# Kernel optimization log

Hardware: AMD Instinct MI355X
Metric: run time of the kernel (lower is better)

Reference implementation:

```python
import jax, jax.numpy as jnp
import numpy as np


def _analytic_phase(x):
    """FFT-based analytic-signal phase, mean over channels. x: (B, C, T) -> (B, T)."""
    B, C, T = x.shape
    Xf = jnp.fft.fft(x, axis=-1)  # complex64
    # Hilbert multiplier: h[0]=1, h[1:T//2]=2, h[T//2]=1 (T even), rest 0
    h = np.zeros((T,), dtype=np.float32)
    h[0] = 1.0
    h[1:T // 2] = 2.0
    if T % 2 == 0:
        h[T // 2] = 1.0
    analytic = jnp.fft.ifft(Xf * jnp.asarray(h), axis=-1)
    phase = jnp.angle(analytic)          # (B, C, T)
    return phase.mean(axis=1)            # (B, T)


def setup_inputs() -> dict:
    key = jax.random.key(0)
    k = jax.random.split(key, 6)
    B, C, T = 32, 9, 4096
    num_codes, code_dim = 512, 64
    half = code_dim // 2
    s = 1.0 / np.sqrt(C)  # kaiming-uniform-ish scale for Linear(9, .)
    return {
        "imu_signal": jax.random.normal(k[0], (B, C, T), dtype=jnp.float32),
        "W_mag": jax.random.uniform(k[1], (half, C), jnp.float32, -s, s),
        "b_mag": jax.random.uniform(k[2], (half,), jnp.float32, -s, s),
        "W_phase": jax.random.uniform(k[3], (half, C), jnp.float32, -s, s),
        "b_phase": jax.random.uniform(k[4], (half,), jnp.float32, -s, s),
        "codebook": jax.random.normal(k[5], (num_codes, code_dim), dtype=jnp.float32),
    }


def reference(imu_signal, W_mag, b_mag, W_phase, b_phase, codebook):
    # imu_signal: (B, 9, T)
    phases = _analytic_phase(imu_signal)                      # (B, T)
    imu_btc = jnp.transpose(imu_signal, (0, 2, 1))            # (B, T, 9)

    mag_features = imu_btc @ W_mag.T + b_mag                  # (B, T, 32)

    phase_input = jnp.stack([jnp.cos(phases), jnp.sin(phases)], axis=-1)  # (B, T, 2)
    combined = jnp.concatenate([imu_btc[:, :, :7], phase_input], axis=-1)  # (B, T, 9)
    phase_features = combined @ W_phase.T + b_phase           # (B, T, 32)

    features = jnp.concatenate([mag_features, phase_features], axis=-1)  # (B, T, 64)

    # cdist argmin == argmin of squared distances: ||f||^2 - 2 f.c + ||c||^2
    d2 = (jnp.sum(features * features, axis=-1, keepdims=True)
          - 2.0 * jnp.einsum("btd,kd->btk", features, codebook)
          + jnp.sum(codebook * codebook, axis=-1))            # (B, T, K)
    indices = jnp.argmin(d2, axis=-1)                         # (B, T)
    quantized = codebook[indices]                             # (B, T, 64)
    return quantized, indices, phases
```

## Files before the change

kernel.cpp:

```cpp
#include <hip/hip_runtime.h>
#include <math.h>

#define TN 4096
#define HN 2048
#define NB 32
#define NCH 9
#define NCODES 512
#define CDIM 64
#define TAU 1e-3f
#define PTS 128
#define CHK 64
#define NCHK 8

typedef _Float16 f16x8 __attribute__((ext_vector_type(8)));
typedef float f32x4 __attribute__((ext_vector_type(4)));

__device__ __forceinline__ float2 cmulf(float2 a, float2 b) {
    return make_float2(a.x * b.x - a.y * b.y, a.x * b.y + a.y * b.x);
}
__device__ __forceinline__ float2 f2add(float2 a, float2 b) {
    return make_float2(a.x + b.x, a.y + b.y);
}
__device__ __forceinline__ float2 f2sub(float2 a, float2 b) {
    return make_float2(a.x - b.x, a.y - b.y);
}

__device__ __forceinline__ unsigned long long packsi(float s, int i) {
    unsigned u = __float_as_uint(s);
    u = (u & 0x80000000u) ? ~u : (u | 0x80000000u);
    return ((unsigned long long)u << 32) | (unsigned)i;
}
__device__ __forceinline__ float unpacks(unsigned long long v) {
    unsigned u = (unsigned)(v >> 32);
    u = (u & 0x80000000u) ? (u & 0x7fffffffu) : ~u;
    return __uint_as_float(u);
}

__device__ __forceinline__ void gload_lds16(const void* g, void* l) {
    __builtin_amdgcn_global_load_lds(
        (const __attribute__((address_space(1))) unsigned int*)g,
        (__attribute__((address_space(3))) unsigned int*)l, 16, 0, 0);
}

__device__ __forceinline__ size_t aunit(int pbase, int plane, int s, int hi16, int l15) {
    return ((size_t)(((pbase * 2 + plane) * 2 + s) * 4 + hi16) << 4) + l15;
}

__global__ __launch_bounds__(256) void prep_kernel(const float* __restrict__ cb,
                                                   float* __restrict__ cn,
                                                   f16x8* __restrict__ cbswz,
                                                   float* __restrict__ ph) {
    const int bid = blockIdx.x;
    const int tid = threadIdx.x;
    if (bid < 512) {
        ph[bid * 256 + tid] = 0.0f;
        return;
    }
    if (bid < 544) {
        const int u = (bid - 512) * 256 + tid;
        const int k = u >> 4;
        const int j = u & 15;
        const int ob = j ^ (k & 15);
        const int plane = ob >> 3;
        const int d0 = (ob & 7) * 8;
        f16x8 out;
        #pragma unroll
        for (int e = 0; e < 8; ++e) {
            float c = cb[k * CDIM + d0 + e];
            _Float16 hh = (_Float16)c;
            out[e] = plane ? (_Float16)(c - (float)hh) : hh;
        }
        cbswz[u] = out;
        return;
    }
    for (int k = tid; k < NCODES; k += 256) {
        const float4* c4 = (const float4*)(cb + (size_t)k * CDIM);
        float s = 0.0f;
        #pragma unroll
        for (int q = 0; q < 16; ++q) {
            float4 c = c4[q];
            s = fmaf(c.x, c.x, s);
            s = fmaf(c.y, c.y, s);
            s = fmaf(c.z, c.z, s);
            s = fmaf(c.w, c.w, s);
        }
        cn[k] = s;
    }
}

#define HT 512
__global__ __launch_bounds__(HT) void hilbert_phase_kernel(
    const float* __restrict__ x, float* __restrict__ phases) {
    __shared__ float2 bufA[TN];
    __shared__ float2 bufB[TN];
    __shared__ float2 tw[HN];
    const int tid = threadIdx.x;
    const int row1 = 2 * blockIdx.x;
    const int row2 = row1 + 1;
    const int b1 = row1 / NCH;
    const int b2 = row2 / NCH;
    const float* xr1 = x + (size_t)row1 * TN;
    const float* xr2 = x + (size_t)row2 * TN;

    for (int i = tid; i < HN; i += HT) {
        float ang = -3.14159265358979323846f * ((float)i / (float)HN);
        float s, c;
        sincosf(ang, &s, &c);
        tw[i] = make_float2(c, s);
    }
    for (int i = tid; i < TN; i += HT) {
        bufA[i] = make_float2(xr1[i], xr2[i]);
    }
    __syncthreads();

    float2* src = bufA;
    float2* dst = bufB;
    for (int stage = 0; stage < 6; ++stage) {
        const int m = 1 << (2 * stage);
        for (int idx = tid; idx < 1024; idx += HT) {
            const int kk = idx & (m - 1);
            const int jm = idx - kk;
            float2 a0 = src[idx];
            float2 a1 = src[idx + 1024];
            float2 a2 = src[idx + 2048];
            float2 a3 = src[idx + 3072];
            float2 b0 = f2add(a0, a2);
            float2 b1 = f2add(a1, a3);
            float2 b2 = f2sub(a0, a2);
            float2 b3 = f2sub(a1, a3);
            float2 w1 = tw[jm];
            float2 w2 = tw[2 * jm];
            float2 w3 = cmulf(w1, w2);
            float2 y0 = f2add(b0, b1);
            float2 mi = make_float2(b2.x + b3.y, b2.y - b3.x);
            float2 pi_ = make_float2(b2.x - b3.y, b2.y + b3.x);
            dst[4 * jm + kk]         = y0;
            dst[4 * jm + kk + m]     = cmulf(mi, w1);
            dst[4 * jm + kk + 2 * m] = cmulf(f2sub(b0, b1), w2);
            dst[4 * jm + kk + 3 * m] = cmulf(pi_, w3);
        }
        __syncthreads();
        float2* t0 = src; src = dst; dst = t0;
    }
    const float inv = 1.0f / (float)TN;
    for (int i = tid; i < TN; i += HT) {
        float sc;
        if (i == 0 || i == HN) sc = inv;
        else if (i < HN) sc = 2.0f * inv;
        else sc = 0.0f;
        float2 v = src[i];
        v.x *= sc; v.y *= sc;
        src[i] = v;
    }
    __syncthreads();
    for (int stage = 0; stage < 6; ++stage) {
        const int m = 1 << (2 * stage);
        for (int idx = tid; idx < 1024; idx += HT) {
            const int kk = idx & (m - 1);
            const int jm = idx - kk;
            float2 a0 = src[idx];
            float2 a1 = src[idx + 1024];
            float2 a2 = src[idx + 2048];
            float2 a3 = src[idx + 3072];
            float2 b0 = f2add(a0, a2);
            float2 b1 = f2add(a1, a3);
            float2 b2 = f2sub(a0, a2);
            float2 b3 = f2sub(a1, a3);
            float2 w1 = tw[jm];      w1.y = -w1.y;
            float2 w2 = tw[2 * jm];  w2.y = -w2.y;
            float2 w3 = cmulf(w1, w2);
            float2 y0 = f2add(b0, b1);
            float2 pi_ = make_float2(b2.x - b3.y, b2.y + b3.x);
            float2 mi = make_float2(b2.x + b3.y, b2.y - b3.x);
            dst[4 * jm + kk]         = y0;
            dst[4 * jm + kk + m]     = cmulf(pi_, w1);
            dst[4 * jm + kk + 2 * m] = cmulf(f2sub(b0, b1), w2);
            dst[4 * jm + kk + 3 * m] = cmulf(mi, w3);
        }
        __syncthreads();
        float2* t0 = src; src = dst; dst = t0;
    }
    float* ph1 = phases + (size_t)b1 * TN;
    float* ph2 = phases + (size_t)b2 * TN;
    for (int i = tid; i < TN; i += HT) {
        float2 d = src[i];
        float x1v = xr1[i];
        float x2v = xr2[i];
        atomicAdd(&ph1[i], atan2f(d.y - x2v, x1v) * (1.0f / 9.0f));
        atomicAdd(&ph2[i], atan2f(x1v - d.x, x2v) * (1.0f / 9.0f));
    }
}

__global__ __launch_bounds__(256) void feat_kernel(
    const float* __restrict__ imu,
    const float* __restrict__ Wm, const float* __restrict__ bm,
    const float* __restrict__ Wp, const float* __restrict__ bp,
    const float* __restrict__ phases,
    f16x8* __restrict__ atiles) {
    const int p = blockIdx.x * 256 + threadIdx.x;
    const int bb = p >> 12;
    const int tt = p & (TN - 1);
    float xc[9];
    #pragma unroll
    for (int c = 0; c < 9; ++c)
        xc[c] = imu[((size_t)(bb * 9 + c)) * TN + tt];
    float sp, cp;
    sincosf(phases[p], &sp, &cp);

    const int pbase = p >> 4;
    const int l15 = p & 15;
    #pragma unroll
    for (int g = 0; g < 8; ++g) {
        float v8[8];
        if (g < 4) {
            #pragma unroll
            for (int e = 0; e < 8; ++e) {
                const int j = 8 * g + e;
                float a = bm[j];
                #pragma unroll
                for (int c = 0; c < 9; ++c) a = fmaf(Wm[j * 9 + c], xc[c], a);
                v8[e] = a;
            }
        } else {
            #pragma unroll
            for (int e = 0; e < 8; ++e) {
                const int j = 8 * (g - 4) + e;
                float a = bp[j];
                #pragma unroll
                for (int c = 0; c < 7; ++c) a = fmaf(Wp[j * 9 + c], xc[c], a);
                a = fmaf(Wp[j * 9 + 7], cp, a);
                a = fmaf(Wp[j * 9 + 8], sp, a);
                v8[e] = a;
            }
        }
        f16x8 hv, lv;
        #pragma unroll
        for (int e = 0; e < 8; ++e) {
            _Float16 hh = (_Float16)v8[e];
            hv[e] = hh;
            lv[e] = (_Float16)(v8[e] - (float)hh);
        }
        const int s = g >> 2;
        const int hi16 = g & 3;
        atiles[aunit(pbase, 0, s, hi16, l15)] = hv;
        atiles[aunit(pbase, 1, s, hi16, l15)] = lv;
    }
}

__global__ __launch_bounds__(256, 2) void vq_kernel(
    const float* __restrict__ imu,
    const float* __restrict__ Wm, const float* __restrict__ bm,
    const float* __restrict__ Wp, const float* __restrict__ bp,
    const float* __restrict__ cb,
    const float* __restrict__ cn,
    const f16x8* __restrict__ cbswz,
    const float* __restrict__ phases,
    const f16x8* atiles,
    float* out_q,
    float* __restrict__ out_i) {
    __shared__ __align__(16) _Float16 sB[2][CHK][128];
    __shared__ int s_idx[PTS];
    const int tid = threadIdx.x;
    const int lane = tid & 63;
    const int w = tid >> 6;
    const int l15 = lane & 15;
    const int hi16 = lane >> 4;
    const int p0 = blockIdx.x * PTS;

    {
        const char* gsrc = (const char*)cbswz;
        char* ldst = (char*)&sB[0][0][0];
        #pragma unroll
        for (int i = 0; i < 4; ++i) {
            const int u = i * 256 + tid;
            gload_lds16(gsrc + (size_t)u * 16, ldst + u * 16);
        }
    }

    f16x8 aH[2][2], aL[2][2];
    #pragma unroll
    for (int rf = 0; rf < 2; ++rf) {
        const int prow = p0 + 32 * w + 16 * rf + l15;
        const int pbase = prow >> 4;
        #pragma unroll
        for (int s = 0; s < 2; ++s) {
            aH[rf][s] = atiles[aunit(pbase, 0, s, hi16, l15)];
            aL[rf][s] = atiles[aunit(pbase, 1, s, hi16, l15)];
        }
    }
    __syncthreads();

    float best[2][4], sec[2][4];
    int bidx[2][4];
    #pragma unroll
    for (int rf = 0; rf < 2; ++rf)
        #pragma unroll
        for (int r = 0; r < 4; ++r) {
            best[rf][r] = 3.4e38f; sec[rf][r] = 3.4e38f; bidx[rf][r] = 0;
        }

    for (int ch = 0; ch < NCHK; ++ch) {
        const int cur = ch & 1;
        if (ch < NCHK - 1) {
            const char* gsrc = (const char*)cbswz + (size_t)(ch + 1) * CHK * 256;
            char* ldst = (char*)&sB[cur ^ 1][0][0];
            #pragma unroll
            for (int i = 0; i < 4; ++i) {
                const int u = i * 256 + tid;
                gload_lds16(gsrc + (size_t)u * 16, ldst + u * 16);
            }
        }
        float cnv[4];
        #pragma unroll
        for (int cf = 0; cf < 4; ++cf) cnv[cf] = cn[ch * CHK + 16 * cf + l15];

        f32x4 acc[2][4];
        #pragma unroll
        for (int rf = 0; rf < 2; ++rf)
            #pragma unroll
            for (int cf = 0; cf < 4; ++cf) acc[rf][cf] = (f32x4){0.f, 0.f, 0.f, 0.f};

        #pragma unroll
        for (int cf = 0; cf < 4; ++cf) {
            const int cl = 16 * cf + l15;
            const f16x8* brow = (const f16x8*)&sB[cur][cl][0];
            #pragma unroll
            for (int s = 0; s < 2; ++s) {
                f16x8 bH = brow[(4 * s + hi16) ^ l15];
                f16x8 bL = brow[(8 + 4 * s + hi16) ^ l15];
                #pragma unroll
                for (int rf = 0; rf < 2; ++rf) {
                    acc[rf][cf] = __builtin_amdgcn_mfma_f32_16x16x32_f16(aH[rf][s], bH, acc[rf][cf], 0, 0, 0);
                    acc[rf][cf] = __builtin_amdgcn_mfma_f32_16x16x32_f16(aH[rf][s], bL, acc[rf][cf], 0, 0, 0);
                    acc[rf][cf] = __builtin_amdgcn_mfma_f32_16x16x32_f16(aL[rf][s], bH, acc[rf][cf], 0, 0, 0);
                }
            }
        }
        #pragma unroll
        for (int cf = 0; cf < 4; ++cf) {
            const int col = ch * CHK + 16 * cf + l15;
            #pragma unroll
            for (int rf = 0; rf < 2; ++rf)
                #pragma unroll
                for (int r = 0; r < 4; ++r) {
                    float sc = fmaf(-2.0f, acc[rf][cf][r], cnv[cf]);
                    bool lt = sc < best[rf][r];
                    float cand = lt ? best[rf][r] : sc;
                    sec[rf][r] = fminf(sec[rf][r], cand);
                    best[rf][r] = fminf(best[rf][r], sc);
                    bidx[rf][r] = lt ? col : bidx[rf][r];
                }
        }
        __syncthreads();
    }

    unsigned long long pb[2][4], ps[2][4];
    #pragma unroll
    for (int rf = 0; rf < 2; ++rf)
        #pragma unroll
        for (int r = 0; r < 4; ++r) {
            pb[rf][r] = packsi(best[rf][r], bidx[rf][r]);
            ps[rf][r] = packsi(sec[rf][r], 0);
        }
    #pragma unroll
    for (int m = 1; m <= 8; m <<= 1) {
        #pragma unroll
        for (int rf = 0; rf < 2; ++rf)
            #pragma unroll
            for (int r = 0; r < 4; ++r) {
                unsigned long long ob = __shfl_xor(pb[rf][r], m, 64);
                unsigned long long os = __shfl_xor(ps[rf][r], m, 64);
                unsigned long long mx = pb[rf][r] > ob ? pb[rf][r] : ob;
                unsigned long long mn = ps[rf][r] < os ? ps[rf][r] : os;
                ps[rf][r] = mx < mn ? mx : mn;
                pb[rf][r] = pb[rf][r] < ob ? pb[rf][r] : ob;
            }
    }
    if (l15 == 0) {
        #pragma unroll
        for (int rf = 0; rf < 2; ++rf)
            #pragma unroll
            for (int r = 0; r < 4; ++r) {
                const int row = 32 * w + 16 * rf + 4 * hi16 + r;
                const int bi = (int)(pb[rf][r] & 0xFFFFFFFFu);
                s_idx[row] = bi;
                out_i[p0 + row] = (float)bi;
            }
    }

    #pragma unroll
    for (int rf = 0; rf < 2; ++rf)
        #pragma unroll
        for (int r = 0; r < 4; ++r) {
            float gap = unpacks(ps[rf][r]) - unpacks(pb[rf][r]);
            unsigned long long bal = __ballot(l15 == 0 && gap < TAU);
            while (bal) {
                const int ln = __builtin_ctzll(bal);
                bal &= bal - 1;
                const int row = 32 * w + 16 * rf + (ln >> 4) * 4 + r;
                const int pR = p0 + row;
                const int bbR = pR >> 12;
                const int ttR = pR & (TN - 1);
                float xcR[9];
                #pragma unroll
                for (int c = 0; c < 9; ++c)
                    xcR[c] = imu[((size_t)(bbR * 9 + c)) * TN + ttR];
                float spR, cpR;
                sincosf(phases[pR], &spR, &cpR);
                float a0[8], a1[8], a2[8], a3[8];
                #pragma unroll
                for (int cc = 0; cc < 8; ++cc) {
                    a0[cc] = 0.f; a1[cc] = 0.f; a2[cc] = 0.f; a3[cc] = 0.f;
                }
                for (int d4 = 0; d4 < 16; ++d4) {
                    float fd[4];
                    #pragma unroll
                    for (int e = 0; e < 4; ++e) {
                        const int j = 4 * d4 + e;
                        float a;
                        if (j < 32) {
                            a = bm[j];
                            #pragma unroll
                            for (int c = 0; c < 9; ++c) a = fmaf(Wm[j * 9 + c], xcR[c], a);
                        } else {
                            const int jj = j - 32;
                            a = bp[jj];
                            #pragma unroll
                            for (int c = 0; c < 7; ++c) a = fmaf(Wp[jj * 9 + c], xcR[c], a);
                            a = fmaf(Wp[jj * 9 + 7], cpR, a);
                            a = fmaf(Wp[jj * 9 + 8], spR, a);
                        }
                        fd[e] = a;
                    }
                    #pragma unroll
                    for (int cc = 0; cc < 8; ++cc) {
                        const float4 cv = ((const float4*)(cb + (size_t)(lane * 8 + cc) * CDIM))[d4];
                        a0[cc] = fmaf(fd[0], cv.x, a0[cc]);
                        a1[cc] = fmaf(fd[1], cv.y, a1[cc]);
                        a2[cc] = fmaf(fd[2], cv.z, a2[cc]);
                        a3[cc] = fmaf(fd[3], cv.w, a3[cc]);
                    }
                }
                unsigned long long pbest = ~0ull;
                #pragma unroll
                for (int cc = 0; cc < 8; ++cc) {
                    const int kk = lane * 8 + cc;
                    float sc = fmaf(-2.0f, (a0[cc] + a1[cc]) + (a2[cc] + a3[cc]), cn[kk]);
                    unsigned long long pk = packsi(sc, kk);
                    pbest = pk < pbest ? pk : pbest;
                }
                #pragma unroll
                for (int m = 1; m <= 32; m <<= 1) {
                    unsigned long long o = __shfl_xor(pbest, m, 64);
                    pbest = o < pbest ? o : pbest;
                }
                if (lane == 0) {
                    const int bi = (int)(pbest & 0xFFFFFFFFu);
                    s_idx[row] = bi;
                    out_i[p0 + row] = (float)bi;
                }
            }
        }
    __syncthreads();

    float4* oq = (float4*)out_q;
    const float4* c4g = (const float4*)cb;
    for (int i = tid; i < PTS * 16; i += 256) {
        const int pt = i >> 4;
        const int q = i & 15;
        oq[(size_t)(p0 + pt) * 16 + q] = c4g[(size_t)s_idx[pt] * 16 + q];
    }
}

extern "C" void kernel_launch(void* const* d_in, const int* in_sizes, int n_in,
                              void* d_out, int out_size, void* d_ws, size_t ws_size,
                              hipStream_t stream) {
    const float* imu = (const float*)d_in[0];
    const float* Wm  = (const float*)d_in[1];
    const float* bm  = (const float*)d_in[2];
    const float* Wp  = (const float*)d_in[3];
    const float* bp  = (const float*)d_in[4];
    const float* cb  = (const float*)d_in[5];

    float* out_q = (float*)d_out;
    float* out_i = out_q + (size_t)NB * TN * CDIM;
    float* out_p = out_i + (size_t)NB * TN;

    float* cn     = (float*)d_ws;
    f16x8* cbswz  = (f16x8*)((char*)d_ws + 2048);
    f16x8* atiles = (f16x8*)out_q;

    prep_kernel<<<545, 256, 0, stream>>>(cb, cn, cbswz, out_p);
    hilbert_phase_kernel<<<NB * NCH / 2, HT, 0, stream>>>(imu, out_p);
    feat_kernel<<<(NB * TN) / 256, 256, 0, stream>>>(imu, Wm, bm, Wp, bp, out_p, atiles);
    vq_kernel<<<(NB * TN) / PTS, 256, 0, stream>>>(imu, Wm, bm, Wp, bp, cb,
                                                   cn, cbswz, out_p, atiles,
                                                   out_q, out_i);
}
```

Measured before the change: 160.1 us.

## Restructure Hilbert FFT per row and enlarge VQ tiles to 512 threads

The Hilbert kernel now handles one channel row per block instead of packing two real rows into one complex FFT. The spectral scaling is folded into the last forward stage, and the first inverse stage skips loads of the zeroed upper half. The VQ kernel moves to 256 points and 128-code chunks per block with 512 threads, and computes accumulators per column fragment so fewer live registers are needed. This doubles the FFT block count and drops the two-for-one real FFT trick. The larger VQ blocks change occupancy, and parts of the VQ indexing that are not shown must agree with the new sizes.

```diff
diff --git a/kernel.cpp b/kernel.cpp
--- a/kernel.cpp
+++ b/kernel.cpp
@@ -8,9 +8,10 @@
 #define NCODES 512
 #define CDIM 64
 #define TAU 1e-3f
-#define PTS 128
-#define CHK 64
-#define NCHK 8
+#define PTS 256
+#define CHK 128
+#define NCHK 4
+#define VQT 512
 
 typedef _Float16 f16x8 __attribute__((ext_vector_type(8)));
 typedef float f32x4 __attribute__((ext_vector_type(4)));
@@ -23,6 +24,9 @@
 }
 __device__ __forceinline__ float2 f2sub(float2 a, float2 b) {
     return make_float2(a.x - b.x, a.y - b.y);
+}
+__device__ __forceinline__ float2 f2scale(float2 a, float s) {
+    return make_float2(a.x * s, a.y * s);
 }
 
 __device__ __forceinline__ unsigned long long packsi(float s, int i) {
@@ -95,12 +99,10 @@
     __shared__ float2 bufB[TN];
     __shared__ float2 tw[HN];
     const int tid = threadIdx.x;
-    const int row1 = 2 * blockIdx.x;
-    const int row2 = row1 + 1;
-    const int b1 = row1 / NCH;
-    const int b2 = row2 / NCH;
-    const float* xr1 = x + (size_t)row1 * TN;
-    const float* xr2 = x + (size_t)row2 * TN;
+    const int row = blockIdx.x;
+    const int b = row / NCH;
+    const float* xr = x + (size_t)row * TN;
+    const float inv = 1.0f / (float)TN;
 
     for (int i = tid; i < HN; i += HT) {
         float ang = -3.14159265358979323846f * ((float)i / (float)HN);
@@ -109,7 +111,7 @@
         tw[i] = make_float2(c, s);
     }
     for (int i = tid; i < TN; i += HT) {
-        bufA[i] = make_float2(xr1[i], xr2[i]);
+        bufA[i] = make_float2(xr[i], 0.0f);
     }
     __syncthreads();
 
@@ -128,31 +130,29 @@
             float2 b1 = f2add(a1, a3);
             float2 b2 = f2sub(a0, a2);
             float2 b3 = f2sub(a1, a3);
-            float2 w1 = tw[jm];
-            float2 w2 = tw[2 * jm];
-            float2 w3 = cmulf(w1, w2);
             float2 y0 = f2add(b0, b1);
             float2 mi = make_float2(b2.x + b3.y, b2.y - b3.x);
             float2 pi_ = make_float2(b2.x - b3.y, b2.y + b3.x);
-            dst[4 * jm + kk]         = y0;
-            dst[4 * jm + kk + m]     = cmulf(mi, w1);
-            dst[4 * jm + kk + 2 * m] = cmulf(f2sub(b0, b1), w2);
-            dst[4 * jm + kk + 3 * m] = cmulf(pi_, w3);
+            if (stage == 5) {
+                const float sA_ = (idx == 0) ? inv : 2.0f * inv;
+                const float sC_ = (idx == 0) ? inv : 0.0f;
+                dst[idx]        = f2scale(y0, sA_);
+                dst[idx + 1024] = f2scale(mi, 2.0f * inv);
+                dst[idx + 2048] = f2scale(f2sub(b0, b1), sC_);
+                dst[idx + 3072] = make_float2(0.0f, 0.0f);
+            } else {
+                float2 w1 = tw[jm];
+                float2 w2 = tw[2 * jm];
+                float2 w3 = cmulf(w1, w2);
+                dst[4 * jm + kk]         = y0;
+                dst[4 * jm + kk + m]     = cmulf(mi, w1);
+                dst[4 * jm + kk + 2 * m] = cmulf(f2sub(b0, b1), w2);
+                dst[4 * jm + kk + 3 * m] = cmulf(pi_, w3);
+            }
         }
         __syncthreads();
         float2* t0 = src; src = dst; dst = t0;
     }
-    const float inv = 1.0f / (float)TN;
-    for (int i = tid; i < TN; i += HT) {
-        float sc;
-        if (i == 0 || i == HN) sc = inv;
-        else if (i < HN) sc = 2.0f * inv;
-        else sc = 0.0f;
-        float2 v = src[i];
-        v.x *= sc; v.y *= sc;
-        src[i] = v;
-    }
-    __syncthreads();
     for (int stage = 0; stage < 6; ++stage) {
         const int m = 1 << (2 * stage);
         for (int idx = tid; idx < 1024; idx += HT) {
@@ -160,8 +160,14 @@
             const int jm = idx - kk;
             float2 a0 = src[idx];
             float2 a1 = src[idx + 1024];
-            float2 a2 = src[idx + 2048];
-            float2 a3 = src[idx + 3072];
+            float2 a2, a3;
+            if (stage == 0) {
+                a2 = (idx == 0) ? src[2048] : make_float2(0.0f, 0.0f);
+                a3 = make_float2(0.0f, 0.0f);
+            } else {
+                a2 = src[idx + 2048];
+                a3 = src[idx + 3072];
+            }
             float2 b0 = f2add(a0, a2);
             float2 b1 = f2add(a1, a3);
             float2 b2 = f2sub(a0, a2);
@@ -180,14 +186,10 @@
         __syncthreads();
         float2* t0 = src; src = dst; dst = t0;
     }
-    float* ph1 = phases + (size_t)b1 * TN;
-    float* ph2 = phases + (size_t)b2 * TN;
+    float* ph = phases + (size_t)b * TN;
     for (int i = tid; i < TN; i += HT) {
-        float2 d = src[i];
-        float x1v = xr1[i];
-        float x2v = xr2[i];
-        atomicAdd(&ph1[i], atan2f(d.y - x2v, x1v) * (1.0f / 9.0f));
-        atomicAdd(&ph2[i], atan2f(x1v - d.x, x2v) * (1.0f / 9.0f));
+        float2 v = src[i];
+        atomicAdd(&ph[i], atan2f(v.y, v.x) * (1.0f / 9.0f));
     }
 }
 
@@ -247,7 +249,7 @@
     }
 }
 
-__global__ __launch_bounds__(256, 2) void vq_kernel(
+__global__ __launch_bounds__(VQT, 4) void vq_kernel(
     const float* __restrict__ imu,
     const float* __restrict__ Wm, const float* __restrict__ bm,
     const float* __restrict__ Wp, const float* __restrict__ bp,
@@ -272,7 +274,7 @@
         char* ldst = (char*)&sB[0][0][0];
         #pragma unroll
         for (int i = 0; i < 4; ++i) {
-            const int u = i * 256 + tid;
+            const int u = i * VQT + tid;
             gload_lds16(gsrc + (size_t)u * 16, ldst + u * 16);
         }
     }
@@ -306,44 +308,36 @@
             char* ldst = (char*)&sB[cur ^ 1][0][0];
             #pragma unroll
             for (int i = 0; i < 4; ++i) {
-                const int u = i * 256 + tid;
+                const int u = i * VQT + tid;
                 gload_lds16(gsrc + (size_t)u * 16, ldst + u * 16);
             }
         }
-        float cnv[4];
-        #pragma unroll
-        for (int cf = 0; cf < 4; ++cf) cnv[cf] = cn[ch * CHK + 16 * cf + l15];
-
-        f32x4 acc[2][4];
-        #pragma unroll
-        for (int rf = 0; rf < 2; ++rf)
-            #pragma unroll
-            for (int cf = 0; cf < 4; ++cf) acc[rf][cf] = (f32x4){0.f, 0.f, 0.f, 0.f};
-
-        #pragma unroll
-        for (int cf = 0; cf < 4; ++cf) {
+
+        #pragma unroll
+        for (int cf = 0; cf < 8; ++cf) {
             const int cl = 16 * cf + l15;
             const f16x8* brow = (const f16x8*)&sB[cur][cl][0];
+            f32x4 acc[2];
+            acc[0] = (f32x4){0.f, 0.f, 0.f, 0.f};
+            acc[1] = (f32x4){0.f, 0.f, 0.f, 0.f};
             #pragma unroll
             for (int s = 0; s < 2; ++s) {
                 f16x8 bH = brow[(4 * s + hi16) ^ l15];
                 f16x8 bL = brow[(8 + 4 * s + hi16) ^ l15];
                 #pragma unroll
                 for (int rf = 0; rf < 2; ++rf) {
-                    acc[rf][cf] = __builtin_amdgcn_mfma_f32_16x16x32_f16(aH[rf][s], bH, acc[rf][cf], 0, 0, 0);
-                    acc[rf][cf] = __builtin_amdgcn_mfma_f32_16x16x32_f16(aH[rf][s], bL, acc[rf][cf], 0, 0, 0);
-                    acc[rf][cf] = __builtin_amdgcn_mfma_f32_16x16x32_f16(aL[rf][s], bH, acc[rf][cf], 0, 0, 0);
-                }
-            }
-        }
-        #pragma unroll
-        for (int cf = 0; cf < 4; ++cf) {
+                    acc[rf] = __builtin_amdgcn_mfma_f32_16x16x32_f16(aH[rf][s], bH, acc[rf], 0, 0, 0);
+                    acc[rf] = __builtin_amdgcn_mfma_f32_16x16x32_f16(aH[rf][s], bL, acc[rf], 0, 0, 0);
+                    acc[rf] = __builtin_amdgcn_mfma_f32_16x16x32_f16(aL[rf][s], bH, acc[rf], 0, 0, 0);
+                }
+            }
             const int col = ch * CHK + 16 * cf + l15;
+            const float cnv = cn[col];
             #pragma unroll
             for (int rf = 0; rf < 2; ++rf)
                 #pragma unroll
                 for (int r = 0; r < 4; ++r) {
-                    float sc = fmaf(-2.0f, acc[rf][cf][r], cnv[cf]);
+                    float sc = fmaf(-2.0f, acc[rf][r], cnv);
                     bool lt = sc < best[rf][r];
                     float cand = lt ? best[rf][r] : sc;
                     sec[rf][r] = fminf(sec[rf][r], cand);
@@ -465,7 +459,7 @@
 
     float4* oq = (float4*)out_q;
     const float4* c4g = (const float4*)cb;
-    for (int i = tid; i < PTS * 16; i += 256) {
+    for (int i = tid; i < PTS * 16; i += VQT) {
         const int pt = i >> 4;
         const int q = i & 15;
         oq[(size_t)(p0 + pt) * 16 + q] = c4g[(size_t)s_idx[pt] * 16 + q];
@@ -491,9 +485,9 @@
     f16x8* atiles = (f16x8*)out_q;
 
     prep_kernel<<<545, 256, 0, stream>>>(cb, cn, cbswz, out_p);
-    hilbert_phase_kernel<<<NB * NCH / 2, HT, 0, stream>>>(imu, out_p);
+    hilbert_phase_kernel<<<NB * NCH, HT, 0, stream>>>(imu, out_p);
     feat_kernel<<<(NB * TN) / 256, 256, 0, stream>>>(imu, Wm, bm, Wp, bp, out_p, atiles);
-    vq_kernel<<<(NB * TN) / PTS, 256, 0, stream>>>(imu, Wm, bm, Wp, bp, cb,
+    vq_kernel<<<(NB * TN) / PTS, VQT, 0, stream>>>(imu, Wm, bm, Wp, bp, cb,
                                                    cn, cbswz, out_p, atiles,
                                                    out_q, out_i);
 }
```

Measured after the change: 172.9 us. 8.0% more time.
